# Optimization experiments

Hardware: AMD Instinct MI355X
Metric: run time of the kernel (lower is better)

## Reference

```python
import jax, jax.numpy as jnp
import numpy as np

B, T, D = 8, 2048, 2048


def setup_inputs() -> dict:
    key = jax.random.key(0)
    ks = jax.random.split(key, 6)
    s = 1.0 / np.sqrt(D)
    return {
        "x": jax.random.normal(ks[0], (B, T, D), dtype=jnp.float32),
        "h_prev": jax.random.normal(ks[1], (B, D), dtype=jnp.float32),
        "Wz": jax.random.uniform(ks[2], (D, D), minval=-s, maxval=s, dtype=jnp.float32),
        "bz": jax.random.uniform(ks[3], (D,), minval=-s, maxval=s, dtype=jnp.float32),
        "Wh": jax.random.uniform(ks[4], (D, D), minval=-s, maxval=s, dtype=jnp.float32),
        "bh": jax.random.uniform(ks[5], (D,), minval=-s, maxval=s, dtype=jnp.float32),
    }


def reference(x, h_prev, Wz, bz, Wh, bh):
    # Batched projections over all timesteps (torch Linear: x @ W.T + b)
    z = jax.nn.sigmoid(jnp.einsum('btd,ed->bte', x, Wz) + bz)  # [B,T,D]
    h_tilde = jnp.einsum('btd,ed->bte', x, Wh) + bh            # [B,T,D]
    # Recurrence h_t = a_t * h_{t-1} + b_t as a parallel associative scan
    a = 1.0 - z
    b = z * h_tilde

    def combine(l, r):
        al, bl = l
        ar, br = r
        return (al * ar, ar * bl + br)

    a_cum, b_cum = jax.lax.associative_scan(combine, (a, b), axis=1)
    out = b_cum + a_cum * h_prev[:, None, :]  # add contribution of initial state
    return out, out[:, -1, :]
```

## Files before the change

### kernel.cpp

```cpp
#include <hip/hip_runtime.h>
#include <hip/hip_bf16.h>
#include <cstdint>

typedef __bf16 bf16_t;
typedef __attribute__((ext_vector_type(8))) __bf16 bf16x8;
typedef __attribute__((ext_vector_type(4))) __bf16 bf16x4;
typedef __attribute__((ext_vector_type(4))) float f32x4;

#define B_ 8
#define T_ 2048
#define D_ 2048
#define M_ (B_ * T_)
#define N2_ (2 * D_)
#define K_ D_

#define BM 128
#define BN 128
#define BK 32
#define NC 32
#define CHUNK (T_ / NC)


__global__ void conv_x_kernel(const float4* __restrict__ in, bf16x4* __restrict__ out, int n4) {
    int i = blockIdx.x * blockDim.x + threadIdx.x;
    if (i >= n4) return;
    float4 v = in[i];
    bf16x4 o = { (bf16_t)v.x, (bf16_t)v.y, (bf16_t)v.z, (bf16_t)v.w };
    out[i] = o;
}

__global__ void conv_w_kernel(const float4* __restrict__ Wz, const float4* __restrict__ Wh,
                              bf16x4* __restrict__ Wb, int n4, int d4) {
    int i = blockIdx.x * blockDim.x + threadIdx.x;
    if (i >= n4) return;
    int row = i / d4;
    int c = i - row * d4;
    float4 vz = Wz[i];
    float4 vh = Wh[i];
    bf16x4 oz = { (bf16_t)vz.x, (bf16_t)vz.y, (bf16_t)vz.z, (bf16_t)vz.w };
    bf16x4 oh = { (bf16_t)vh.x, (bf16_t)vh.y, (bf16_t)vh.z, (bf16_t)vh.w };
    Wb[(size_t)(2 * row) * d4 + c] = oz;
    Wb[(size_t)(2 * row + 1) * d4 + c] = oh;
}


__device__ __forceinline__ void gload_lds16(const void* g, void* l) {
    __builtin_amdgcn_global_load_lds(
        (__attribute__((address_space(1))) void*)(g),
        (__attribute__((address_space(3))) void*)(l), 16, 0, 0);
}

__global__ __launch_bounds__(256, 2) void gemm_fused(
    const bf16_t* __restrict__ Xb,
    const bf16_t* __restrict__ Wb,
    const float* __restrict__ bz, const float* __restrict__ bh,
    bf16_t* __restrict__ Aco,
    bf16_t* __restrict__ Bco)
{
    __shared__ bf16_t sA[BM * BK];
    __shared__ bf16_t sB[BN * BK];

    const int t = threadIdx.x;
    const int wave = t >> 6, lane = t & 63;
    const int wr = wave >> 1, wc = wave & 1;
    const int bm0 = blockIdx.y * BM;
    const int bn0 = blockIdx.x * BN;

    const int srow = t >> 2;
    const int scol = (t & 3) * 8;
    const bf16_t* gA = Xb + (size_t)(bm0 + srow) * K_ + scol;
    const bf16_t* gB = Wb + (size_t)(bn0 + srow) * K_ + scol;

    const int fr = lane & 15;
    const int kg = (lane >> 4) * 8;

    f32x4 acc[4][4] = {};

    for (int k0 = 0; k0 < K_; k0 += BK) {
#pragma unroll
        for (int j = 0; j < 2; ++j) {
            gload_lds16(gA + (size_t)(j * 64) * K_ + k0,
                        (char*)sA + j * 4096 + wave * 1024);
            gload_lds16(gB + (size_t)(j * 64) * K_ + k0,
                        (char*)sB + j * 4096 + wave * 1024);
        }
        __syncthreads();

        bf16x8 av[4], bv[4];
#pragma unroll
        for (int mi = 0; mi < 4; ++mi)
            av[mi] = *(const bf16x8*)&sA[(wr * 64 + mi * 16 + fr) * BK + kg];
#pragma unroll
        for (int ni = 0; ni < 4; ++ni)
            bv[ni] = *(const bf16x8*)&sB[(wc * 64 + ni * 16 + fr) * BK + kg];

#pragma unroll
        for (int mi = 0; mi < 4; ++mi)
#pragma unroll
            for (int ni = 0; ni < 4; ++ni)
                acc[mi][ni] = __builtin_amdgcn_mfma_f32_16x16x32_bf16(
                    av[mi], bv[ni], acc[mi][ni], 0, 0, 0);
        __syncthreads();
    }

    const int rquad = (lane >> 4) * 4;
#pragma unroll
    for (int mi = 0; mi < 4; ++mi) {
#pragma unroll
        for (int ni = 0; ni < 4; ++ni) {
#pragma unroll
            for (int r = 0; r < 4; ++r) {
                float v = acc[mi][ni][r];
                float other = __shfl_xor(v, 1);
                int m = bm0 + wr * 64 + mi * 16 + rquad + r;
                int n2 = bn0 + wc * 64 + ni * 16 + fr;
                int ch = n2 >> 1;
                float zraw = (lane & 1) ? other : v;
                float z = 1.0f / (1.0f + __expf(-(zraw + bz[ch])));
                if (lane & 1) {
                    float hv = v + bh[ch];
                    Bco[(size_t)m * D_ + ch] = (bf16_t)(z * hv);
                } else {
                    Aco[(size_t)m * D_ + ch] = (bf16_t)(1.0f - z);
                }
            }
        }
    }
}


__global__ void scan_chunk_summary(const bf16_t* __restrict__ Aco, const bf16_t* __restrict__ Bco,
                                   float* __restrict__ cA, float* __restrict__ cB) {
    int d = blockIdx.x * blockDim.x + threadIdx.x;
    int c = blockIdx.y, bb = blockIdx.z;
    size_t base = ((size_t)bb * T_ + (size_t)c * CHUNK) * D_ + d;
    float A = 1.0f, Bv = 0.0f;
#pragma unroll 4
    for (int tt = 0; tt < CHUNK; ++tt) {
        float a = (float)Aco[base + (size_t)tt * D_];
        float b = (float)Bco[base + (size_t)tt * D_];
        A *= a;
        Bv = a * Bv + b;
    }
    size_t ci = ((size_t)bb * NC + c) * D_ + d;
    cA[ci] = A;
    cB[ci] = Bv;
}

__global__ void scan_carry(const float* __restrict__ cA, const float* __restrict__ cB,
                           const float* __restrict__ h_prev, float* __restrict__ carry) {
    int idx = blockIdx.x * blockDim.x + threadIdx.x;
    int bb = idx / D_, d = idx - bb * D_;
    float h = h_prev[idx];
    for (int c = 0; c < NC; ++c) {
        size_t ci = ((size_t)bb * NC + c) * D_ + d;
        carry[ci] = h;
        h = cA[ci] * h + cB[ci];
    }
}

__global__ void scan_apply(const bf16_t* __restrict__ Aco, const bf16_t* __restrict__ Bco,
                           const float* __restrict__ carry, float* __restrict__ out,
                           float* __restrict__ last) {
    int d = blockIdx.x * blockDim.x + threadIdx.x;
    int c = blockIdx.y, bb = blockIdx.z;
    size_t ci = ((size_t)bb * NC + c) * D_ + d;
    float h = carry[ci];
    size_t base = ((size_t)bb * T_ + (size_t)c * CHUNK) * D_ + d;
    for (int tt = 0; tt < CHUNK; ++tt) {
        float a = (float)Aco[base + (size_t)tt * D_];
        float b = (float)Bco[base + (size_t)tt * D_];
        h = a * h + b;
        out[base + (size_t)tt * D_] = h;
    }
    if (c == NC - 1) last[(size_t)bb * D_ + d] = h;
}


extern "C" void kernel_launch(void* const* d_in, const int* in_sizes, int n_in,
                              void* d_out, int out_size, void* d_ws, size_t ws_size,
                              hipStream_t stream) {
    const float* x      = (const float*)d_in[0];
    const float* h_prev = (const float*)d_in[1];
    const float* Wz     = (const float*)d_in[2];
    const float* bz     = (const float*)d_in[3];
    const float* Wh     = (const float*)d_in[4];
    const float* bh     = (const float*)d_in[5];

    float* out  = (float*)d_out;
    float* last = out + (size_t)M_ * D_;

    char* ws = (char*)d_ws;
    bf16_t* Xb  = (bf16_t*)ws;
    bf16_t* Wb  = (bf16_t*)(ws + (size_t)M_ * K_ * 2);
    bf16_t* Aco = (bf16_t*)((char*)Wb + (size_t)N2_ * K_ * 2);
    bf16_t* Bco = Aco + (size_t)M_ * D_;
    float*  cA  = (float*)((char*)Bco + (size_t)M_ * D_ * 2);
    float*  cB  = cA + (size_t)B_ * NC * D_;
    float*  carry = cB + (size_t)B_ * NC * D_;

    {
        int n4 = M_ * K_ / 4;
        conv_x_kernel<<<(n4 + 255) / 256, 256, 0, stream>>>((const float4*)x, (bf16x4*)Xb, n4);
    }
    {
        int n4 = D_ * D_ / 4;
        conv_w_kernel<<<(n4 + 255) / 256, 256, 0, stream>>>((const float4*)Wz, (const float4*)Wh,
                                                            (bf16x4*)Wb, n4, D_ / 4);
    }
    gemm_fused<<<dim3(N2_ / BN, M_ / BM), 256, 0, stream>>>(Xb, Wb, bz, bh, Aco, Bco);
    scan_chunk_summary<<<dim3(D_ / 256, NC, B_), 256, 0, stream>>>(Aco, Bco, cA, cB);
    scan_carry<<<(B_ * D_) / 256, 256, 0, stream>>>(cA, cB, h_prev, carry);
    scan_apply<<<dim3(D_ / 256, NC, B_), 256, 0, stream>>>(Aco, Bco, carry, out, last);
}
```

Baseline: 675.4 us.

## Rewrite GEMM as 256x256 tile with double-buffered LDS, XOR swizzle, and priority pipelining

Replaces the 128x128x32 single-buffer GEMM with a 256x256 tile per 512-thread block, BK=64, and 128KB of double-buffered LDS. Global-to-LDS loads for the next k-step are interleaved with MFMA phases using explicit waitcnt, barriers and s_setprio. An XOR swizzle on LDS chunks is meant to avoid bank conflicts. Bias loads are hoisted out of the epilogue. The larger tile improves data reuse and hides load latency, but the heavy LDS use and register pressure limit occupancy, and the hand-written sync ordering is fragile.

```diff
diff --git a/kernel.cpp b/kernel.cpp
--- a/kernel.cpp
+++ b/kernel.cpp
@@ -13,12 +13,14 @@
 #define M_ (B_ * T_)
 #define N2_ (2 * D_)
 #define K_ D_
-
-#define BM 128
-#define BN 128
-#define BK 32
+#define NT (K_ / 64)
+
 #define NC 32
 #define CHUNK (T_ / NC)
+
+#define BAR() __builtin_amdgcn_s_barrier()
+#define WAIT_LGKM0() asm volatile("s_waitcnt lgkmcnt(0)" ::: "memory")
+#define WAIT_VM(n) asm volatile("s_waitcnt vmcnt(" #n ")" ::: "memory")
 
 
 __global__ void conv_x_kernel(const float4* __restrict__ in, bf16x4* __restrict__ out, int n4) {
@@ -44,82 +46,166 @@
 }
 
 
-__device__ __forceinline__ void gload_lds16(const void* g, void* l) {
+__device__ __forceinline__ void gload_lds16(const bf16_t* g, char* l) {
     __builtin_amdgcn_global_load_lds(
         (__attribute__((address_space(1))) void*)(g),
         (__attribute__((address_space(3))) void*)(l), 16, 0, 0);
 }
 
-__global__ __launch_bounds__(256, 2) void gemm_fused(
+
+__global__ __launch_bounds__(512, 2) void gemm_fused(
     const bf16_t* __restrict__ Xb,
     const bf16_t* __restrict__ Wb,
     const float* __restrict__ bz, const float* __restrict__ bh,
     bf16_t* __restrict__ Aco,
     bf16_t* __restrict__ Bco)
 {
-    __shared__ bf16_t sA[BM * BK];
-    __shared__ bf16_t sB[BN * BK];
+    __shared__ __attribute__((aligned(16))) char lds[131072];
 
     const int t = threadIdx.x;
     const int wave = t >> 6, lane = t & 63;
-    const int wr = wave >> 1, wc = wave & 1;
-    const int bm0 = blockIdx.y * BM;
-    const int bn0 = blockIdx.x * BN;
-
-    const int srow = t >> 2;
-    const int scol = (t & 3) * 8;
-    const bf16_t* gA = Xb + (size_t)(bm0 + srow) * K_ + scol;
-    const bf16_t* gB = Wb + (size_t)(bn0 + srow) * K_ + scol;
-
-    const int fr = lane & 15;
-    const int kg = (lane >> 4) * 8;
-
-    f32x4 acc[4][4] = {};
-
-    for (int k0 = 0; k0 < K_; k0 += BK) {
-#pragma unroll
-        for (int j = 0; j < 2; ++j) {
-            gload_lds16(gA + (size_t)(j * 64) * K_ + k0,
-                        (char*)sA + j * 4096 + wave * 1024);
-            gload_lds16(gB + (size_t)(j * 64) * K_ + k0,
-                        (char*)sB + j * 4096 + wave * 1024);
-        }
-        __syncthreads();
-
-        bf16x8 av[4], bv[4];
-#pragma unroll
-        for (int mi = 0; mi < 4; ++mi)
-            av[mi] = *(const bf16x8*)&sA[(wr * 64 + mi * 16 + fr) * BK + kg];
-#pragma unroll
-        for (int ni = 0; ni < 4; ++ni)
-            bv[ni] = *(const bf16x8*)&sB[(wc * 64 + ni * 16 + fr) * BK + kg];
-
-#pragma unroll
-        for (int mi = 0; mi < 4; ++mi)
-#pragma unroll
-            for (int ni = 0; ni < 4; ++ni)
-                acc[mi][ni] = __builtin_amdgcn_mfma_f32_16x16x32_bf16(
-                    av[mi], bv[ni], acc[mi][ni], 0, 0, 0);
-        __syncthreads();
-    }
-
-    const int rquad = (lane >> 4) * 4;
-#pragma unroll
-    for (int mi = 0; mi < 4; ++mi) {
+    const int wr = wave >> 2, wc = wave & 3;
+    const int fr = lane & 15, ln4 = lane >> 4;
+    const int fr7 = fr & 7;
+    const int bn0 = blockIdx.x * 256;
+    const int bm0 = blockIdx.y * 256;
+
+    const int l3 = lane >> 3, l7 = lane & 7;
+    const int schunk = (l7 ^ l3) * 8;
+    const int srow = wave * 8 + l3;
+
+    const int csA[2] = { ((0 + ln4) ^ fr7) * 16, ((4 + ln4) ^ fr7) * 16 };
+    const int rbaseA = wr * 16384 + fr * 128;
+    const int rbaseB = wc * 8192 + fr * 128;
+
+    auto stageA = [&](int buf, int h, int u) {
+        const bf16_t* g = Xb + (size_t)(bm0 + h * 128 + srow) * K_ + u * 64 + schunk;
+        char* l0 = lds + buf * 65536 + h * 16384 + wave * 1024;
+        gload_lds16(g, l0);
+        gload_lds16(g + (size_t)64 * K_, l0 + 8192);
+    };
+    auto stageB = [&](int buf, int h, int u) {
+        const bf16_t* g = Wb + (size_t)(bn0 + h * 128 + srow) * K_ + u * 64 + schunk;
+        char* l0 = lds + buf * 65536 + 32768 + h * 16384 + wave * 1024;
+        gload_lds16(g, l0);
+        gload_lds16(g + (size_t)64 * K_, l0 + 8192);
+    };
+
+#define RD_A(p, mi, kh) (*(const bf16x8*)(lds + (p) * 65536 + rbaseA + (mi) * 2048 + csA[kh]))
+#define RD_B(p, ni, kh) (*(const bf16x8*)(lds + (p) * 65536 + 32768 + rbaseB + (ni) * 2048 + csA[kh]))
+
+    f32x4 acc[8][4] = {};
+    bf16x8 afr[4][2], bfr[4][2];
+
+    stageA(0, 0, 0); stageA(0, 1, 0); stageB(0, 0, 0); stageB(0, 1, 0);
+    stageA(1, 0, 1); stageA(1, 1, 1);
+    WAIT_VM(4);
+    BAR();
+
+    for (int u = 0; u < NT; ++u) {
+        const int p = u & 1;
+
+#pragma unroll
+        for (int mi = 0; mi < 4; ++mi)
+#pragma unroll
+            for (int kh = 0; kh < 2; ++kh)
+                afr[mi][kh] = RD_A(p, mi, kh);
+#pragma unroll
+        for (int ni = 0; ni < 2; ++ni)
+#pragma unroll
+            for (int kh = 0; kh < 2; ++kh)
+                bfr[ni][kh] = RD_B(p, ni, kh);
+        if (u + 1 < NT) stageB(p ^ 1, 0, u + 1);
+        BAR();
+        __builtin_amdgcn_s_setprio(1);
+#pragma unroll
+        for (int mi = 0; mi < 4; ++mi)
+#pragma unroll
+            for (int ni = 0; ni < 2; ++ni)
+#pragma unroll
+                for (int kh = 0; kh < 2; ++kh)
+                    acc[mi][ni] = __builtin_amdgcn_mfma_f32_16x16x32_bf16(
+                        afr[mi][kh], bfr[ni][kh], acc[mi][ni], 0, 0, 0);
+        __builtin_amdgcn_s_setprio(0);
+        BAR();
+
+#pragma unroll
+        for (int ni = 2; ni < 4; ++ni)
+#pragma unroll
+            for (int kh = 0; kh < 2; ++kh)
+                bfr[ni][kh] = RD_B(p, ni, kh);
+        if (u + 1 < NT) stageB(p ^ 1, 1, u + 1);
+        BAR();
+        __builtin_amdgcn_s_setprio(1);
+#pragma unroll
+        for (int mi = 0; mi < 4; ++mi)
+#pragma unroll
+            for (int ni = 2; ni < 4; ++ni)
+#pragma unroll
+                for (int kh = 0; kh < 2; ++kh)
+                    acc[mi][ni] = __builtin_amdgcn_mfma_f32_16x16x32_bf16(
+                        afr[mi][kh], bfr[ni][kh], acc[mi][ni], 0, 0, 0);
+        __builtin_amdgcn_s_setprio(0);
+        BAR();
+
+#pragma unroll
+        for (int mi = 0; mi < 4; ++mi)
+#pragma unroll
+            for (int kh = 0; kh < 2; ++kh)
+                afr[mi][kh] = RD_A(p, mi + 4, kh);
+        WAIT_LGKM0();
+        BAR();
+        if (u + 2 < NT) stageA(p, 0, u + 2);
+        __builtin_amdgcn_s_setprio(1);
+#pragma unroll
+        for (int mi = 0; mi < 4; ++mi)
+#pragma unroll
+            for (int ni = 0; ni < 2; ++ni)
+#pragma unroll
+                for (int kh = 0; kh < 2; ++kh)
+                    acc[mi + 4][ni] = __builtin_amdgcn_mfma_f32_16x16x32_bf16(
+                        afr[mi][kh], bfr[ni][kh], acc[mi + 4][ni], 0, 0, 0);
+        __builtin_amdgcn_s_setprio(0);
+        BAR();
+
+        if (u + 2 < NT) stageA(p, 1, u + 2);
+        __builtin_amdgcn_s_setprio(1);
+#pragma unroll
+        for (int mi = 0; mi < 4; ++mi)
+#pragma unroll
+            for (int ni = 2; ni < 4; ++ni)
+#pragma unroll
+                for (int kh = 0; kh < 2; ++kh)
+                    acc[mi + 4][ni] = __builtin_amdgcn_mfma_f32_16x16x32_bf16(
+                        afr[mi][kh], bfr[ni][kh], acc[mi + 4][ni], 0, 0, 0);
+        __builtin_amdgcn_s_setprio(0);
+        if (u < NT - 2)       { WAIT_VM(4); }
+        else if (u == NT - 2) { WAIT_VM(0); }
+        BAR();
+    }
+
+    float bzv[4], bhv[4];
+#pragma unroll
+    for (int ni = 0; ni < 4; ++ni) {
+        int ch = (bn0 + wc * 64 + ni * 16 + fr) >> 1;
+        bzv[ni] = bz[ch];
+        bhv[ni] = bh[ch];
+    }
+#pragma unroll
+    for (int mi = 0; mi < 8; ++mi) {
 #pragma unroll
         for (int ni = 0; ni < 4; ++ni) {
 #pragma unroll
-            for (int r = 0; r < 4; ++r) {
-                float v = acc[mi][ni][r];
+            for (int q = 0; q < 4; ++q) {
+                float v = acc[mi][ni][q];
                 float other = __shfl_xor(v, 1);
-                int m = bm0 + wr * 64 + mi * 16 + rquad + r;
+                int m = bm0 + wr * 128 + mi * 16 + ln4 * 4 + q;
                 int n2 = bn0 + wc * 64 + ni * 16 + fr;
                 int ch = n2 >> 1;
                 float zraw = (lane & 1) ? other : v;
-                float z = 1.0f / (1.0f + __expf(-(zraw + bz[ch])));
+                float z = 1.0f / (1.0f + __expf(-(zraw + bzv[ni])));
                 if (lane & 1) {
-                    float hv = v + bh[ch];
-                    Bco[(size_t)m * D_ + ch] = (bf16_t)(z * hv);
+                    Bco[(size_t)m * D_ + ch] = (bf16_t)(z * (v + bhv[ni]));
                 } else {
                     Aco[(size_t)m * D_ + ch] = (bf16_t)(1.0f - z);
                 }
@@ -208,7 +294,7 @@
         conv_w_kernel<<<(n4 + 255) / 256, 256, 0, stream>>>((const float4*)Wz, (const float4*)Wh,
                                                             (bf16x4*)Wb, n4, D_ / 4);
     }
-    gemm_fused<<<dim3(N2_ / BN, M_ / BM), 256, 0, stream>>>(Xb, Wb, bz, bh, Aco, Bco);
+    gemm_fused<<<dim3(N2_ / 256, M_ / 256), 512, 0, stream>>>(Xb, Wb, bz, bh, Aco, Bco);
     scan_chunk_summary<<<dim3(D_ / 256, NC, B_), 256, 0, stream>>>(Aco, Bco, cA, cB);
     scan_carry<<<(B_ * D_) / 256, 256, 0, stream>>>(cA, cB, h_prev, carry);
     scan_apply<<<dim3(D_ / 256, NC, B_), 256, 0, stream>>>(Aco, Bco, carry, out, last);
```

Measured after the change: 596.6 us. -11.7%, faster.
